# Optimization experiments

Measured on AMD Instinct MI355X. Metric: run time of the kernel, lower is better.

## Reference

```python
import jax, jax.numpy as jnp
import numpy as np

B, N, D, H = 4, 2048, 512, 8
HD = D // H  # 64


def setup_inputs() -> dict:
    key = jax.random.key(0)
    ks = jax.random.split(key, 12)
    s = 0.02
    return {
        "x": jax.random.normal(ks[0], (B, N, D), jnp.float32),
        "freqs": jax.random.normal(ks[1], (B, N, HD // 2), jnp.float32),
        # weights stored as (in, out); torch Linear applies x @ W.T + b
        "wqkv_w": jax.random.normal(ks[2], (D, 3 * D), jnp.float32) * s,
        "wqkv_b": jax.random.normal(ks[3], (3 * D,), jnp.float32) * s,
        "out_w": jax.random.normal(ks[4], (D, D), jnp.float32) * s,
        "out_b": jax.random.normal(ks[5], (D,), jnp.float32) * s,
        "ffn1_w": jax.random.normal(ks[6], (2 * D, 2 * D), jnp.float32) * s,
        "ffn1_b": jax.random.normal(ks[7], (2 * D,), jnp.float32) * s,
        "ln_g": jnp.ones((2 * D,), jnp.float32),
        "ln_b": jnp.zeros((2 * D,), jnp.float32),
        "ffn2_w": jax.random.normal(ks[8], (2 * D, D), jnp.float32) * s,
        "ffn2_b": jax.random.normal(ks[9], (D,), jnp.float32) * s,
    }


def _rope(t, cos, sin):
    # t: [B,H,N,HD]; cos/sin: [B,1,N,HD/2]
    x1, x2 = t[..., ::2], t[..., 1::2]
    return jnp.stack([x1 * cos - x2 * sin, x1 * sin + x2 * cos], axis=-1).reshape(t.shape)


def reference(x, freqs, wqkv_w, wqkv_b, out_w, out_b,
              ffn1_w, ffn1_b, ln_g, ln_b, ffn2_w, ffn2_b):
    b, n, d = x.shape
    h, hd = H, d // H
    qkv = x @ wqkv_w + wqkv_b                      # [B,N,3D]
    q, k, v = jnp.split(qkv, 3, axis=-1)
    to_heads = lambda t: t.reshape(b, n, h, hd).transpose(0, 2, 1, 3)  # [B,H,N,HD]
    q, k, v = to_heads(q), to_heads(k), to_heads(v)
    cos = jnp.cos(freqs)[:, None]                  # [B,1,N,HD/2]
    sin = jnp.sin(freqs)[:, None]
    q = _rope(q, cos, sin)
    k = _rope(k, cos, sin)
    scale = hd ** -0.5
    attn = jax.nn.softmax(jnp.einsum('bhqd,bhkd->bhqk', q, k) * scale, axis=-1)
    msg = jnp.einsum('bhqk,bhkd->bhqd', attn, v).transpose(0, 2, 1, 3).reshape(b, n, d)
    msg = msg @ out_w + out_b
    # FFN on concat([x, msg]): Linear -> LayerNorm -> GELU(exact) -> Linear
    hcat = jnp.concatenate([x, msg], axis=-1) @ ffn1_w + ffn1_b   # [B,N,2D]
    mu = hcat.mean(-1, keepdims=True)
    var = hcat.var(-1, keepdims=True)
    hcat = (hcat - mu) * jax.lax.rsqrt(var + 1e-5) * ln_g + ln_b
    hcat = jax.nn.gelu(hcat, approximate=False)
    return x + hcat @ ffn2_w + ffn2_b
```

## Files before the change

### kernel.cpp

```cpp
#include <hip/hip_runtime.h>
#include <hip/hip_bf16.h>
#include <math.h>

typedef __bf16 bf16;
typedef __bf16 bf16x2 __attribute__((ext_vector_type(2)));
typedef __bf16 bf16x4 __attribute__((ext_vector_type(4)));
typedef __bf16 bf16x8 __attribute__((ext_vector_type(8)));
typedef float f32x4 __attribute__((ext_vector_type(4)));
typedef float f32x16 __attribute__((ext_vector_type(16)));

#define MFMA16(a, b, c) __builtin_amdgcn_mfma_f32_16x16x32_bf16(a, b, c, 0, 0, 0)
#define MFMA32(a, b, c) __builtin_amdgcn_mfma_f32_32x32x16_bf16(a, b, c, 0, 0, 0)


__global__ __launch_bounds__(256) void transpose_all_kernel(
    const float* __restrict__ w0, const float* __restrict__ w1,
    const float* __restrict__ w2, const float* __restrict__ w3,
    bf16* __restrict__ d0, bf16* __restrict__ d1,
    bf16* __restrict__ d2, bf16* __restrict__ d3)
{
    const int bid = blockIdx.x;
    const float* src; bf16* dst; int R, C, bx, by;
    if (bid < 768)       { src = w0; dst = d0; R = 512;  C = 1536; int r = bid;        bx = r % 48; by = r / 48; }
    else if (bid < 1024) { src = w1; dst = d1; R = 512;  C = 512;  int r = bid - 768;  bx = r % 16; by = r / 16; }
    else if (bid < 2048) { src = w2; dst = d2; R = 1024; C = 1024; int r = bid - 1024; bx = r % 32; by = r / 32; }
    else                 { src = w3; dst = d3; R = 1024; C = 512;  int r = bid - 2048; bx = r % 16; by = r / 16; }
    __shared__ bf16 tile[32][33];
    const int tx = threadIdx.x & 31, ty = threadIdx.x >> 5;
    const int x = bx * 32 + tx;
#pragma unroll
    for (int j = 0; j < 4; j++)
        tile[ty + 8 * j][tx] = (bf16)src[(size_t)(by * 32 + ty + 8 * j) * C + x];
    __syncthreads();
    const int x2 = by * 32 + tx;
#pragma unroll
    for (int j = 0; j < 4; j++)
        dst[(size_t)(bx * 32 + ty + 8 * j) * R + x2] = tile[tx][ty + 8 * j];
}

__global__ __launch_bounds__(256) void cast_x_kernel(const float* __restrict__ x,
                                                     bf16* __restrict__ cat)
{
    int i = blockIdx.x * 256 + threadIdx.x;
    int row = i >> 7, col = (i & 127) << 2;
    const float4 v = *(const float4*)(&x[(size_t)row * 512 + col]);
    bf16x4 o; o[0] = (bf16)v.x; o[1] = (bf16)v.y; o[2] = (bf16)v.z; o[3] = (bf16)v.w;
    *(bf16x4*)(&cat[(size_t)row * 1024 + col]) = o;
}

__global__ __launch_bounds__(256) void rope_kernel(bf16* __restrict__ qb,
                                                   bf16* __restrict__ kb,
                                                   const float* __restrict__ freqs)
{
    const float SC = 0.125f * 1.44269504089f;
    const int bh = blockIdx.x >> 6, nblk = blockIdx.x & 63;
    const int g = threadIdx.x & 7, nl = threadIdx.x >> 3;
    const int n = nblk * 32 + nl;
    const int b = bh >> 3;
    const float4 f = *(const float4*)(&freqs[((size_t)b * 2048 + n) * 32 + g * 4]);
    const float cs[4] = {cosf(f.x), cosf(f.y), cosf(f.z), cosf(f.w)};
    const float sn[4] = {sinf(f.x), sinf(f.y), sinf(f.z), sinf(f.w)};
    const size_t off = ((size_t)bh * 2048 + n) * 64 + g * 8;
    bf16x8 q8 = *(bf16x8*)(qb + off);
    bf16x8 k8 = *(bf16x8*)(kb + off);
#pragma unroll
    for (int i = 0; i < 4; i++) {
        float q1 = q8[2 * i], q2 = q8[2 * i + 1];
        q8[2 * i]     = (bf16)((q1 * cs[i] - q2 * sn[i]) * SC);
        q8[2 * i + 1] = (bf16)((q1 * sn[i] + q2 * cs[i]) * SC);
        float k1 = k8[2 * i], k2 = k8[2 * i + 1];
        k8[2 * i]     = (bf16)(k1 * cs[i] - k2 * sn[i]);
        k8[2 * i + 1] = (bf16)(k1 * sn[i] + k2 * cs[i]);
    }
    *(bf16x8*)(qb + off) = q8;
    *(bf16x8*)(kb + off) = k8;
}

template <int MODE>
__global__ __launch_bounds__(256) void gemm_mfma(
    const bf16* __restrict__ A, int lda, const bf16* __restrict__ Bt,
    const float* __restrict__ bias, void* __restrict__ outv,
    const float* __restrict__ auxf, bf16* __restrict__ o1, bf16* __restrict__ o2,
    int K)
{
    const int tid = threadIdx.x;
    const int lane = tid & 63;
    const int wave = tid >> 6;
    const int wm = wave >> 1, wn = wave & 1;
    const int l15 = lane & 15, quad = lane >> 4;
    const int m0 = blockIdx.y * 128;
    const int n0 = blockIdx.x * 128;

    __shared__ bf16 As[128 * 32];
    __shared__ bf16 Bs[128 * 32];

    const int c0 = tid, c1 = tid + 256;
    const int r0 = c0 >> 2, kc0 = (c0 & 3) << 3;
    const int r1 = c1 >> 2, kc1 = (c1 & 3) << 3;

    const bf16* pA0 = &A[(size_t)(m0 + r0) * lda + kc0];
    const bf16* pA1 = &A[(size_t)(m0 + r1) * lda + kc1];
    const bf16* pB0 = &Bt[(size_t)(n0 + r0) * K + kc0];
    const bf16* pB1 = &Bt[(size_t)(n0 + r1) * K + kc1];

    const f32x4 zero = {0.f, 0.f, 0.f, 0.f};
    f32x4 acc[4][4];
#pragma unroll
    for (int i = 0; i < 4; i++)
#pragma unroll
        for (int j = 0; j < 4; j++) acc[i][j] = zero;

    bf16x8 ra0 = *(const bf16x8*)pA0;
    bf16x8 ra1 = *(const bf16x8*)pA1;
    bf16x8 rb0 = *(const bf16x8*)pB0;
    bf16x8 rb1 = *(const bf16x8*)pB1;

    for (int k0 = 0; k0 < K; k0 += 32) {
        __syncthreads();
        *(bf16x8*)(&As[c0 * 8]) = ra0;
        *(bf16x8*)(&As[c1 * 8]) = ra1;
        *(bf16x8*)(&Bs[c0 * 8]) = rb0;
        *(bf16x8*)(&Bs[c1 * 8]) = rb1;
        __syncthreads();
        if (k0 + 32 < K) {
            ra0 = *(const bf16x8*)(pA0 + k0 + 32);
            ra1 = *(const bf16x8*)(pA1 + k0 + 32);
            rb0 = *(const bf16x8*)(pB0 + k0 + 32);
            rb1 = *(const bf16x8*)(pB1 + k0 + 32);
        }
        bf16x8 af[4], bfv[4];
#pragma unroll
        for (int t = 0; t < 4; t++) {
            af[t]  = *(const bf16x8*)(&As[(wm * 64 + t * 16 + l15) * 32 + quad * 8]);
            bfv[t] = *(const bf16x8*)(&Bs[(wn * 64 + t * 16 + l15) * 32 + quad * 8]);
        }
#pragma unroll
        for (int mt = 0; mt < 4; mt++)
#pragma unroll
            for (int nt = 0; nt < 4; nt++)
                acc[mt][nt] = MFMA16(af[mt], bfv[nt], acc[mt][nt]);
    }

    const int row_base = m0 + wm * 64;
    const int col_base = n0 + wn * 64;

    if constexpr (MODE == 0) {
        const int sector = col_base >> 9;
        bf16* dstbase = (sector == 0) ? (bf16*)outv : (sector == 1 ? o1 : o2);
#pragma unroll
        for (int nt = 0; nt < 4; nt++) {
            const int col = col_base + nt * 16 + l15;
            const int cq = col & 511;
            const int h = cq >> 6, hd = cq & 63;
            const float bv = bias[col];
#pragma unroll
            for (int mt = 0; mt < 4; mt++) {
#pragma unroll
                for (int r = 0; r < 4; r++) {
                    const int mrow = row_base + mt * 16 + quad * 4 + r;
                    const int b = mrow >> 11, n = mrow & 2047;
                    dstbase[(((size_t)b * 8 + h) * 2048 + n) * 64 + hd] =
                        (bf16)(acc[mt][nt][r] + bv);
                }
            }
        }
    } else {
#pragma unroll
        for (int nt = 0; nt < 4; nt++) {
            const int col = col_base + nt * 16 + l15;
            const float bv = bias[col];
#pragma unroll
            for (int mt = 0; mt < 4; mt++) {
#pragma unroll
                for (int r = 0; r < 4; r++) {
                    const int row = row_base + mt * 16 + quad * 4 + r;
                    float v = acc[mt][nt][r] + bv;
                    if constexpr (MODE == 1) {
                        ((bf16*)outv)[(size_t)row * 1024 + 512 + col] = (bf16)v;
                    } else if constexpr (MODE == 2) {
                        ((bf16*)outv)[(size_t)row * 1024 + col] = (bf16)v;
                    } else {
                        v += auxf[(size_t)row * 512 + col];
                        ((float*)outv)[(size_t)row * 512 + col] = v;
                    }
                }
            }
        }
    }
}

__global__ __launch_bounds__(256) void attn_kernel(const bf16* __restrict__ qb,
                                                   const bf16* __restrict__ kb,
                                                   const bf16* __restrict__ vb,
                                                   bf16* __restrict__ ao)
{
    __shared__ bf16 Ks[128 * 72];
    __shared__ bf16 Vts[64 * 136];

    const int tid = threadIdx.x, lane = tid & 63, wave = tid >> 6;
    const int l31 = lane & 31, half = lane >> 5;
    const int bh = blockIdx.x >> 4, qt = blockIdx.x & 15;
    const int b = bh >> 3, h = bh & 7;
    const size_t base = (size_t)bh * 2048 * 64;
    const int m0 = qt * 128 + wave * 32;

    bf16x8 aq[4];
#pragma unroll
    for (int k4 = 0; k4 < 4; k4++)
        aq[k4] = *(const bf16x8*)(&qb[base + (size_t)(m0 + l31) * 64 + k4 * 16 + half * 8]);

    f32x16 accO[2];
#pragma unroll
    for (int i = 0; i < 16; i++) { accO[0][i] = 0.f; accO[1][i] = 0.f; }
    float lsum = 0.f;

    int krow[4], kcol[4], vpr[2], vdg[2];
#pragma unroll
    for (int i = 0; i < 4; i++) { int c = tid + i * 256; krow[i] = c >> 3; kcol[i] = (c & 7) << 3; }
#pragma unroll
    for (int i = 0; i < 2; i++) { int t = tid + i * 256; vpr[i] = t & 63; vdg[i] = t >> 6; }

    bf16x8 kreg[4], vreg0[2], vreg1[2];
    auto prefetch = [&](int key0) {
#pragma unroll
        for (int i = 0; i < 4; i++)
            kreg[i] = *(const bf16x8*)(&kb[base + (size_t)(key0 + krow[i]) * 64 + kcol[i]]);
#pragma unroll
        for (int i = 0; i < 2; i++) {
            vreg0[i] = *(const bf16x8*)(&vb[base + (size_t)(key0 + 2 * vpr[i]) * 64 + vdg[i] * 8]);
            vreg1[i] = *(const bf16x8*)(&vb[base + (size_t)(key0 + 2 * vpr[i] + 1) * 64 + vdg[i] * 8]);
        }
    };

    prefetch(0);
    for (int kt = 0; kt < 16; kt++) {
        __syncthreads();
#pragma unroll
        for (int i = 0; i < 4; i++)
            *(bf16x8*)(&Ks[krow[i] * 72 + kcol[i]]) = kreg[i];
#pragma unroll
        for (int i = 0; i < 2; i++) {
#pragma unroll
            for (int j = 0; j < 8; j++) {
                bf16x2 pr; pr[0] = vreg0[i][j]; pr[1] = vreg1[i][j];
                *(bf16x2*)(&Vts[(vdg[i] * 8 + j) * 136 + 2 * vpr[i]]) = pr;
            }
        }
        __syncthreads();
        if (kt < 15) prefetch((kt + 1) * 128);

#pragma unroll
        for (int nb = 0; nb < 4; nb++) {
            const int ko = nb * 32;
            f32x16 s;
#pragma unroll
            for (int i = 0; i < 16; i++) s[i] = 0.f;
#pragma unroll
            for (int k4 = 0; k4 < 4; k4++) {
                bf16x8 ak = *(const bf16x8*)(&Ks[(ko + l31) * 72 + k4 * 16 + half * 8]);
                s = MFMA32(ak, aq[k4], s);
            }
            float p[16];
#pragma unroll
            for (int r = 0; r < 16; r++) p[r] = exp2f(s[r]);
            lsum += (((p[0] + p[1]) + (p[2] + p[3])) + ((p[4] + p[5]) + (p[6] + p[7])))
                  + (((p[8] + p[9]) + (p[10] + p[11])) + ((p[12] + p[13]) + (p[14] + p[15])));
            unsigned pk[8];
#pragma unroll
            for (int i2 = 0; i2 < 8; i2++) {
                union { bf16x2 hh; unsigned u; } t;
                t.hh[0] = (bf16)p[2 * i2]; t.hh[1] = (bf16)p[2 * i2 + 1];
                pk[i2] = t.u;
            }
            const unsigned sa = half ? pk[0] : pk[2];
            const unsigned sb = half ? pk[1] : pk[3];
            const unsigned sc2 = half ? pk[4] : pk[6];
            const unsigned sd = half ? pk[5] : pk[7];
            const unsigned ra = (unsigned)__shfl_xor((int)sa, 32);
            const unsigned rb = (unsigned)__shfl_xor((int)sb, 32);
            const unsigned rc = (unsigned)__shfl_xor((int)sc2, 32);
            const unsigned rd = (unsigned)__shfl_xor((int)sd, 32);
            union { bf16x8 v; unsigned u[4]; } B0, B1;
            B0.u[0] = half ? ra : pk[0];
            B0.u[1] = half ? rb : pk[1];
            B0.u[2] = half ? pk[2] : ra;
            B0.u[3] = half ? pk[3] : rb;
            B1.u[0] = half ? rc : pk[4];
            B1.u[1] = half ? rd : pk[5];
            B1.u[2] = half ? pk[6] : rc;
            B1.u[3] = half ? pk[7] : rd;
#pragma unroll
            for (int dh = 0; dh < 2; dh++) {
                bf16x8 av0 = *(const bf16x8*)(&Vts[(dh * 32 + l31) * 136 + ko + half * 8]);
                bf16x8 av1 = *(const bf16x8*)(&Vts[(dh * 32 + l31) * 136 + ko + 16 + half * 8]);
                accO[dh] = MFMA32(av0, B0.v, accO[dh]);
                accO[dh] = MFMA32(av1, B1.v, accO[dh]);
            }
        }
    }

    lsum += __shfl_xor(lsum, 32);
    const float inv = 1.0f / lsum;

    const int n = m0 + l31;
    bf16* aor = ao + ((size_t)b * 2048 + n) * 512 + h * 64;
#pragma unroll
    for (int dh = 0; dh < 2; dh++) {
#pragma unroll
        for (int g = 0; g < 4; g++) {
            bf16x4 o4;
#pragma unroll
            for (int e = 0; e < 4; e++) o4[e] = (bf16)(accO[dh][g * 4 + e] * inv);
            *(bf16x4*)(&aor[dh * 32 + g * 8 + half * 4]) = o4;
        }
    }
}

__global__ __launch_bounds__(256) void ln_gelu_kernel(bf16* __restrict__ hb,
                                                      const float* __restrict__ g,
                                                      const float* __restrict__ bt)
{
    const int row = blockIdx.x, tid = threadIdx.x;
    const int lane = tid & 63, wave = tid >> 6;
    bf16* hr = hb + (size_t)row * 1024;
    bf16x4 hv = *(const bf16x4*)(&hr[tid * 4]);
    float v0 = hv[0], v1 = hv[1], v2 = hv[2], v3 = hv[3];
    float s = v0 + v1 + v2 + v3;
    float q = v0 * v0 + v1 * v1 + v2 * v2 + v3 * v3;
    for (int o = 32; o; o >>= 1) { s += __shfl_xor(s, o); q += __shfl_xor(q, o); }
    __shared__ float red[8];
    if (lane == 0) { red[wave] = s; red[4 + wave] = q; }
    __syncthreads();
    s = red[0] + red[1] + red[2] + red[3];
    q = red[4] + red[5] + red[6] + red[7];
    const float mu = s * (1.f / 1024.f);
    const float rstd = rsqrtf(q * (1.f / 1024.f) - mu * mu + 1e-5f);
    const float4 gv = *(const float4*)(&g[tid * 4]);
    const float4 bv = *(const float4*)(&bt[tid * 4]);
    float vv[4] = {v0, v1, v2, v3};
    const float gg[4] = {gv.x, gv.y, gv.z, gv.w};
    const float bb[4] = {bv.x, bv.y, bv.z, bv.w};
    bf16x4 o4;
#pragma unroll
    for (int i = 0; i < 4; i++) {
        float y = (vv[i] - mu) * rstd * gg[i] + bb[i];
        float ge = 0.5f * y * (1.0f + erff(y * 0.70710678118f));
        o4[i] = (bf16)ge;
    }
    *(bf16x4*)(&hr[tid * 4]) = o4;
}

extern "C" void kernel_launch(void* const* d_in, const int* in_sizes, int n_in,
                              void* d_out, int out_size, void* d_ws, size_t ws_size,
                              hipStream_t stream) {
    (void)in_sizes; (void)n_in; (void)out_size; (void)ws_size;
    const float* x      = (const float*)d_in[0];
    const float* freqs  = (const float*)d_in[1];
    const float* wqkv_w = (const float*)d_in[2];
    const float* wqkv_b = (const float*)d_in[3];
    const float* out_w  = (const float*)d_in[4];
    const float* out_b  = (const float*)d_in[5];
    const float* ffn1_w = (const float*)d_in[6];
    const float* ffn1_b = (const float*)d_in[7];
    const float* ln_g   = (const float*)d_in[8];
    const float* ln_b   = (const float*)d_in[9];
    const float* ffn2_w = (const float*)d_in[10];
    const float* ffn2_b = (const float*)d_in[11];
    float* out = (float*)d_out;
    bf16* ws   = (bf16*)d_ws;

    bf16* wqkv_t = ws;
    bf16* out_t  = wqkv_t + 1536 * 512;
    bf16* ffn1_t = out_t + 512 * 512;
    bf16* ffn2_t = ffn1_t + 1024 * 1024;
    bf16* cat    = ffn2_t + 512 * 1024;
    bf16* qbuf   = cat + (size_t)8192 * 1024;
    bf16* kbuf   = qbuf + (size_t)8192 * 512;
    bf16* vbuf   = kbuf + (size_t)8192 * 512;
    bf16* aobuf  = vbuf + (size_t)8192 * 512;
    bf16* hbuf   = qbuf;

    transpose_all_kernel<<<2560, 256, 0, stream>>>(wqkv_w, out_w, ffn1_w, ffn2_w,
                                                   wqkv_t, out_t, ffn1_t, ffn2_t);
    cast_x_kernel<<<4096, 256, 0, stream>>>(x, cat);

    gemm_mfma<0><<<dim3(12, 64), 256, 0, stream>>>(cat, 1024, wqkv_t, wqkv_b, qbuf, nullptr, kbuf, vbuf, 512);
    rope_kernel<<<2048, 256, 0, stream>>>(qbuf, kbuf, freqs);
    attn_kernel<<<512, 256, 0, stream>>>(qbuf, kbuf, vbuf, aobuf);
    gemm_mfma<1><<<dim3(4, 64), 256, 0, stream>>>(aobuf, 512, out_t, out_b, cat, nullptr, nullptr, nullptr, 512);
    gemm_mfma<2><<<dim3(8, 64), 256, 0, stream>>>(cat, 1024, ffn1_t, ffn1_b, hbuf, nullptr, nullptr, nullptr, 1024);
    ln_gelu_kernel<<<8192, 256, 0, stream>>>(hbuf, ln_g, ln_b);
    gemm_mfma<3><<<dim3(4, 64), 256, 0, stream>>>(hbuf, 1024, ffn2_t, ffn2_b, out, x, nullptr, nullptr, 1024);
}
```

Measured before the change: 266.3 us.

## Fold out-projection into FFN1 weights, fuse RoPE into QKV epilogue, split attention keys

Precomputes the product of the output projection and the lower half of ffn1 weights (plus a fused bias) so the activation out-projection GEMM is eliminated and attention writes straight into the concat buffer. RoPE with the softmax scale is applied inside the QKV GEMM epilogue via lane shuffles, removing the separate rope pass. Attention blocks grow to 512 threads with two waves per query group splitting keys and reducing through shared memory. Weight prep and x cast are merged into one launch; sin/cos are recomputed per element in the epilogue and bf16 rounding of the fused weight changes numerics slightly.

```diff
diff --git a/kernel.cpp b/kernel.cpp
--- a/kernel.cpp
+++ b/kernel.cpp
@@ -13,67 +13,64 @@
 #define MFMA32(a, b, c) __builtin_amdgcn_mfma_f32_32x32x16_bf16(a, b, c, 0, 0, 0)
 
 
-__global__ __launch_bounds__(256) void transpose_all_kernel(
-    const float* __restrict__ w0, const float* __restrict__ w1,
-    const float* __restrict__ w2, const float* __restrict__ w3,
-    bf16* __restrict__ d0, bf16* __restrict__ d1,
-    bf16* __restrict__ d2, bf16* __restrict__ d3)
+__global__ __launch_bounds__(256) void prep_kernel(
+    const float* __restrict__ wqkv_w, const float* __restrict__ out_w,
+    const float* __restrict__ ffn1_w, const float* __restrict__ ffn2_w,
+    const float* __restrict__ x,
+    bf16* __restrict__ wqkv_t, bf16* __restrict__ ffn2_t,
+    bf16* __restrict__ fused_t, bf16* __restrict__ ffn1bt,
+    bf16* __restrict__ out_cast, bf16* __restrict__ cat)
 {
-    const int bid = blockIdx.x;
-    const float* src; bf16* dst; int R, C, bx, by;
-    if (bid < 768)       { src = w0; dst = d0; R = 512;  C = 1536; int r = bid;        bx = r % 48; by = r / 48; }
-    else if (bid < 1024) { src = w1; dst = d1; R = 512;  C = 512;  int r = bid - 768;  bx = r % 16; by = r / 16; }
-    else if (bid < 2048) { src = w2; dst = d2; R = 1024; C = 1024; int r = bid - 1024; bx = r % 32; by = r / 32; }
-    else                 { src = w3; dst = d3; R = 1024; C = 512;  int r = bid - 2048; bx = r % 16; by = r / 16; }
+    const int bid = blockIdx.x, tid = threadIdx.x;
+    if (bid >= 2560) {
+        int i = (bid - 2560) * 256 + tid;
+        int row = i >> 7, col = (i & 127) << 2;
+        const float4 v = *(const float4*)(&x[(size_t)row * 512 + col]);
+        bf16x4 o; o[0] = (bf16)v.x; o[1] = (bf16)v.y; o[2] = (bf16)v.z; o[3] = (bf16)v.w;
+        *(bf16x4*)(&cat[(size_t)row * 1024 + col]) = o;
+        return;
+    }
+    if (bid >= 2304) {
+        int i = (bid - 2304) * 1024 + tid * 4;
+        const float4 v = *(const float4*)(&out_w[i]);
+        bf16x4 o; o[0] = (bf16)v.x; o[1] = (bf16)v.y; o[2] = (bf16)v.z; o[3] = (bf16)v.w;
+        *(bf16x4*)(&out_cast[i]) = o;
+        return;
+    }
+    const float* src; bf16* dst; int C, ldd, bx, by;
+    if (bid < 768)       { src = wqkv_w;            dst = wqkv_t;  C = 1536; ldd = 512;  int r = bid;        bx = r % 48; by = r / 48; }
+    else if (bid < 1280) { src = ffn2_w;            dst = ffn2_t;  C = 512;  ldd = 1024; int r = bid - 768;  bx = r % 16; by = r / 16; }
+    else if (bid < 1792) { src = ffn1_w;            dst = fused_t; C = 1024; ldd = 1024; int r = bid - 1280; bx = r % 32; by = r / 32; }
+    else                 { src = ffn1_w + 512*1024; dst = ffn1bt;  C = 1024; ldd = 512;  int r = bid - 1792; bx = r % 32; by = r / 32; }
     __shared__ bf16 tile[32][33];
-    const int tx = threadIdx.x & 31, ty = threadIdx.x >> 5;
-    const int x = bx * 32 + tx;
+    const int tx = tid & 31, ty = tid >> 5;
+    const int xx = bx * 32 + tx;
 #pragma unroll
     for (int j = 0; j < 4; j++)
-        tile[ty + 8 * j][tx] = (bf16)src[(size_t)(by * 32 + ty + 8 * j) * C + x];
+        tile[ty + 8 * j][tx] = (bf16)src[(size_t)(by * 32 + ty + 8 * j) * C + xx];
     __syncthreads();
     const int x2 = by * 32 + tx;
 #pragma unroll
     for (int j = 0; j < 4; j++)
-        dst[(size_t)(bx * 32 + ty + 8 * j) * R + x2] = tile[tx][ty + 8 * j];
-}
-
-__global__ __launch_bounds__(256) void cast_x_kernel(const float* __restrict__ x,
-                                                     bf16* __restrict__ cat)
+        dst[(size_t)(bx * 32 + ty + 8 * j) * ldd + x2] = tile[tx][ty + 8 * j];
+}
+
+__global__ __launch_bounds__(256) void bias_fuse_kernel(
+    const float* __restrict__ ffn1_w, const float* __restrict__ ffn1_b,
+    const float* __restrict__ out_b, float* __restrict__ bias_f)
 {
-    int i = blockIdx.x * 256 + threadIdx.x;
-    int row = i >> 7, col = (i & 127) << 2;
-    const float4 v = *(const float4*)(&x[(size_t)row * 512 + col]);
-    bf16x4 o; o[0] = (bf16)v.x; o[1] = (bf16)v.y; o[2] = (bf16)v.z; o[3] = (bf16)v.w;
-    *(bf16x4*)(&cat[(size_t)row * 1024 + col]) = o;
-}
-
-__global__ __launch_bounds__(256) void rope_kernel(bf16* __restrict__ qb,
-                                                   bf16* __restrict__ kb,
-                                                   const float* __restrict__ freqs)
-{
-    const float SC = 0.125f * 1.44269504089f;
-    const int bh = blockIdx.x >> 6, nblk = blockIdx.x & 63;
-    const int g = threadIdx.x & 7, nl = threadIdx.x >> 3;
-    const int n = nblk * 32 + nl;
-    const int b = bh >> 3;
-    const float4 f = *(const float4*)(&freqs[((size_t)b * 2048 + n) * 32 + g * 4]);
-    const float cs[4] = {cosf(f.x), cosf(f.y), cosf(f.z), cosf(f.w)};
-    const float sn[4] = {sinf(f.x), sinf(f.y), sinf(f.z), sinf(f.w)};
-    const size_t off = ((size_t)bh * 2048 + n) * 64 + g * 8;
-    bf16x8 q8 = *(bf16x8*)(qb + off);
-    bf16x8 k8 = *(bf16x8*)(kb + off);
-#pragma unroll
-    for (int i = 0; i < 4; i++) {
-        float q1 = q8[2 * i], q2 = q8[2 * i + 1];
-        q8[2 * i]     = (bf16)((q1 * cs[i] - q2 * sn[i]) * SC);
-        q8[2 * i + 1] = (bf16)((q1 * sn[i] + q2 * cs[i]) * SC);
-        float k1 = k8[2 * i], k2 = k8[2 * i + 1];
-        k8[2 * i]     = (bf16)(k1 * cs[i] - k2 * sn[i]);
-        k8[2 * i + 1] = (bf16)(k1 * sn[i] + k2 * cs[i]);
-    }
-    *(bf16x8*)(qb + off) = q8;
-    *(bf16x8*)(kb + off) = k8;
+    __shared__ float red[256];
+    const int t = threadIdx.x;
+    const int n = blockIdx.x * 64 + (t & 63);
+    const int ic = t >> 6;
+    float acc = 0.f;
+#pragma unroll 8
+    for (int i = ic * 128; i < ic * 128 + 128; i++)
+        acc += out_b[i] * ffn1_w[(size_t)(512 + i) * 1024 + n];
+    red[t] = acc;
+    __syncthreads();
+    if (t < 64)
+        bias_f[n] = ffn1_b[n] + red[t] + red[t + 64] + red[t + 128] + red[t + 192];
 }
 
 template <int MODE>
@@ -145,6 +142,7 @@
     const int col_base = n0 + wn * 64;
 
     if constexpr (MODE == 0) {
+        const float SCQ = 0.125f * 1.44269504089f;
         const int sector = col_base >> 9;
         bf16* dstbase = (sector == 0) ? (bf16*)outv : (sector == 1 ? o1 : o2);
 #pragma unroll
@@ -153,14 +151,24 @@
             const int cq = col & 511;
             const int h = cq >> 6, hd = cq & 63;
             const float bv = bias[col];
+            const int ihalf = hd >> 1;
+            const bool odd = (hd & 1) != 0;
 #pragma unroll
             for (int mt = 0; mt < 4; mt++) {
 #pragma unroll
                 for (int r = 0; r < 4; r++) {
                     const int mrow = row_base + mt * 16 + quad * 4 + r;
+                    float v = acc[mt][nt][r] + bv;
+                    float o = v;
+                    if (sector < 2) {
+                        float p = __shfl_xor(v, 1);
+                        float fr = auxf[(size_t)mrow * 32 + ihalf];
+                        float cs = cosf(fr), sn = sinf(fr);
+                        o = odd ? (p * sn + v * cs) : (v * cs - p * sn);
+                        if (sector == 0) o *= SCQ;
+                    }
                     const int b = mrow >> 11, n = mrow & 2047;
-                    dstbase[(((size_t)b * 8 + h) * 2048 + n) * 64 + hd] =
-                        (bf16)(acc[mt][nt][r] + bv);
+                    dstbase[(((size_t)b * 8 + h) * 2048 + n) * 64 + hd] = (bf16)o;
                 }
             }
         }
@@ -168,20 +176,21 @@
 #pragma unroll
         for (int nt = 0; nt < 4; nt++) {
             const int col = col_base + nt * 16 + l15;
-            const float bv = bias[col];
+            float bv = 0.f;
+            if constexpr (MODE != 4) bv = bias[col];
 #pragma unroll
             for (int mt = 0; mt < 4; mt++) {
 #pragma unroll
                 for (int r = 0; r < 4; r++) {
                     const int row = row_base + mt * 16 + quad * 4 + r;
                     float v = acc[mt][nt][r] + bv;
-                    if constexpr (MODE == 1) {
-                        ((bf16*)outv)[(size_t)row * 1024 + 512 + col] = (bf16)v;
-                    } else if constexpr (MODE == 2) {
+                    if constexpr (MODE == 2) {
                         ((bf16*)outv)[(size_t)row * 1024 + col] = (bf16)v;
-                    } else {
+                    } else if constexpr (MODE == 3) {
                         v += auxf[(size_t)row * 512 + col];
                         ((float*)outv)[(size_t)row * 512 + col] = v;
+                    } else {
+                        ((bf16*)outv)[(size_t)row * 1024 + 512 + col] = (bf16)v;
                     }
                 }
             }
@@ -189,20 +198,22 @@
     }
 }
 
-__global__ __launch_bounds__(256) void attn_kernel(const bf16* __restrict__ qb,
+__global__ __launch_bounds__(512) void attn_kernel(const bf16* __restrict__ qb,
                                                    const bf16* __restrict__ kb,
                                                    const bf16* __restrict__ vb,
-                                                   bf16* __restrict__ ao)
+                                                   bf16* __restrict__ cat)
 {
-    __shared__ bf16 Ks[128 * 72];
-    __shared__ bf16 Vts[64 * 136];
+    __shared__ __align__(16) char smem[35840];
+    bf16* Ks  = (bf16*)smem;
+    bf16* Vts = (bf16*)(smem + 128 * 72 * 2);
 
     const int tid = threadIdx.x, lane = tid & 63, wave = tid >> 6;
     const int l31 = lane & 31, half = lane >> 5;
+    const int qg = wave >> 1, kh = wave & 1;
     const int bh = blockIdx.x >> 4, qt = blockIdx.x & 15;
     const int b = bh >> 3, h = bh & 7;
     const size_t base = (size_t)bh * 2048 * 64;
-    const int m0 = qt * 128 + wave * 32;
+    const int m0 = qt * 128 + qg * 32;
 
     bf16x8 aq[4];
 #pragma unroll
@@ -214,44 +225,37 @@
     for (int i = 0; i < 16; i++) { accO[0][i] = 0.f; accO[1][i] = 0.f; }
     float lsum = 0.f;
 
-    int krow[4], kcol[4], vpr[2], vdg[2];
-#pragma unroll
-    for (int i = 0; i < 4; i++) { int c = tid + i * 256; krow[i] = c >> 3; kcol[i] = (c & 7) << 3; }
-#pragma unroll
-    for (int i = 0; i < 2; i++) { int t = tid + i * 256; vpr[i] = t & 63; vdg[i] = t >> 6; }
-
-    bf16x8 kreg[4], vreg0[2], vreg1[2];
+    int krow[2], kcol[2];
+#pragma unroll
+    for (int i = 0; i < 2; i++) { int c = tid + i * 512; krow[i] = c >> 3; kcol[i] = (c & 7) << 3; }
+    const int vpr = tid & 63, vdg = tid >> 6;
+
+    bf16x8 kreg[2], vr0, vr1;
     auto prefetch = [&](int key0) {
 #pragma unroll
-        for (int i = 0; i < 4; i++)
+        for (int i = 0; i < 2; i++)
             kreg[i] = *(const bf16x8*)(&kb[base + (size_t)(key0 + krow[i]) * 64 + kcol[i]]);
-#pragma unroll
-        for (int i = 0; i < 2; i++) {
-            vreg0[i] = *(const bf16x8*)(&vb[base + (size_t)(key0 + 2 * vpr[i]) * 64 + vdg[i] * 8]);
-            vreg1[i] = *(const bf16x8*)(&vb[base + (size_t)(key0 + 2 * vpr[i] + 1) * 64 + vdg[i] * 8]);
-        }
+        vr0 = *(const bf16x8*)(&vb[base + (size_t)(key0 + 2 * vpr) * 64 + vdg * 8]);
+        vr1 = *(const bf16x8*)(&vb[base + (size_t)(key0 + 2 * vpr + 1) * 64 + vdg * 8]);
     };
 
     prefetch(0);
     for (int kt = 0; kt < 16; kt++) {
         __syncthreads();
 #pragma unroll
-        for (int i = 0; i < 4; i++)
+        for (int i = 0; i < 2; i++)
             *(bf16x8*)(&Ks[krow[i] * 72 + kcol[i]]) = kreg[i];
 #pragma unroll
-        for (int i = 0; i < 2; i++) {
-#pragma unroll
-            for (int j = 0; j < 8; j++) {
-                bf16x2 pr; pr[0] = vreg0[i][j]; pr[1] = vreg1[i][j];
-                *(bf16x2*)(&Vts[(vdg[i] * 8 + j) * 136 + 2 * vpr[i]]) = pr;
-            }
+        for (int j = 0; j < 8; j++) {
+            bf16x2 pr; pr[0] = vr0[j]; pr[1] = vr1[j];
+            *(bf16x2*)(&Vts[(vdg * 8 + j) * 136 + 2 * vpr]) = pr;
         }
         __syncthreads();
         if (kt < 15) prefetch((kt + 1) * 128);
 
 #pragma unroll
-        for (int nb = 0; nb < 4; nb++) {
-            const int ko = nb * 32;
+        for (int nb = 0; nb < 2; nb++) {
+            const int ko = kh * 64 + nb * 32;
             f32x16 s;
 #pragma unroll
             for (int i = 0; i < 16; i++) s[i] = 0.f;
@@ -299,19 +303,31 @@
         }
     }
 
-    lsum += __shfl_xor(lsum, 32);
-    const float inv = 1.0f / lsum;
-
-    const int n = m0 + l31;
-    bf16* aor = ao + ((size_t)b * 2048 + n) * 512 + h * 64;
-#pragma unroll
-    for (int dh = 0; dh < 2; dh++) {
-#pragma unroll
-        for (int g = 0; g < 4; g++) {
-            bf16x4 o4;
-#pragma unroll
-            for (int e = 0; e < 4; e++) o4[e] = (bf16)(accO[dh][g * 4 + e] * inv);
-            *(bf16x4*)(&aor[dh * 32 + g * 8 + half * 4]) = o4;
+    __syncthreads();
+    float* red = (float*)smem + qg * 2112 + lane * 33;
+    if (kh == 1) {
+#pragma unroll
+        for (int dh = 0; dh < 2; dh++)
+#pragma unroll
+            for (int r = 0; r < 16; r++) red[dh * 16 + r] = accO[dh][r];
+        red[32] = lsum + __shfl_xor(lsum, 32);
+    }
+    __syncthreads();
+    if (kh == 0) {
+        const float lm = lsum + __shfl_xor(lsum, 32) + red[32];
+        const float inv = 1.0f / lm;
+        const int n = m0 + l31;
+        bf16* aor = cat + ((size_t)b * 2048 + n) * 1024 + 512 + h * 64;
+#pragma unroll
+        for (int dh = 0; dh < 2; dh++) {
+#pragma unroll
+            for (int g = 0; g < 4; g++) {
+                bf16x4 o4;
+#pragma unroll
+                for (int e = 0; e < 4; e++)
+                    o4[e] = (bf16)((accO[dh][g * 4 + e] + red[dh * 16 + g * 4 + e]) * inv);
+                *(bf16x4*)(&aor[dh * 32 + g * 8 + half * 4]) = o4;
+            }
         }
     }
 }
@@ -369,26 +385,26 @@
     float* out = (float*)d_out;
     bf16* ws   = (bf16*)d_ws;
 
-    bf16* wqkv_t = ws;
-    bf16* out_t  = wqkv_t + 1536 * 512;
-    bf16* ffn1_t = out_t + 512 * 512;
-    bf16* ffn2_t = ffn1_t + 1024 * 1024;
-    bf16* cat    = ffn2_t + 512 * 1024;
-    bf16* qbuf   = cat + (size_t)8192 * 1024;
-    bf16* kbuf   = qbuf + (size_t)8192 * 512;
-    bf16* vbuf   = kbuf + (size_t)8192 * 512;
-    bf16* aobuf  = vbuf + (size_t)8192 * 512;
-    bf16* hbuf   = qbuf;
-
-    transpose_all_kernel<<<2560, 256, 0, stream>>>(wqkv_w, out_w, ffn1_w, ffn2_w,
-                                                   wqkv_t, out_t, ffn1_t, ffn2_t);
-    cast_x_kernel<<<4096, 256, 0, stream>>>(x, cat);
-
-    gemm_mfma<0><<<dim3(12, 64), 256, 0, stream>>>(cat, 1024, wqkv_t, wqkv_b, qbuf, nullptr, kbuf, vbuf, 512);
-    rope_kernel<<<2048, 256, 0, stream>>>(qbuf, kbuf, freqs);
-    attn_kernel<<<512, 256, 0, stream>>>(qbuf, kbuf, vbuf, aobuf);
-    gemm_mfma<1><<<dim3(4, 64), 256, 0, stream>>>(aobuf, 512, out_t, out_b, cat, nullptr, nullptr, nullptr, 512);
-    gemm_mfma<2><<<dim3(8, 64), 256, 0, stream>>>(cat, 1024, ffn1_t, ffn1_b, hbuf, nullptr, nullptr, nullptr, 1024);
+    bf16* wqkv_t   = ws;
+    bf16* ffn2_t   = wqkv_t + 1536 * 512;
+    bf16* fused_t  = ffn2_t + 512 * 1024;
+    bf16* ffn1bt   = fused_t + 1024 * 1024;
+    bf16* out_cast = ffn1bt + 1024 * 512;
+    bf16* cat      = out_cast + 512 * 512;
+    bf16* qbuf     = cat + (size_t)8192 * 1024;
+    bf16* kbuf     = qbuf + (size_t)8192 * 512;
+    bf16* vbuf     = kbuf + (size_t)8192 * 512;
+    float* bias_f  = (float*)(vbuf + (size_t)8192 * 512);
+    bf16* hbuf     = qbuf;
+
+    prep_kernel<<<6656, 256, 0, stream>>>(wqkv_w, out_w, ffn1_w, ffn2_w, x,
+                                          wqkv_t, ffn2_t, fused_t, ffn1bt, out_cast, cat);
+    bias_fuse_kernel<<<16, 256, 0, stream>>>(ffn1_w, ffn1_b, out_b, bias_f);
+    gemm_mfma<4><<<dim3(4, 8), 256, 0, stream>>>(ffn1bt, 512, out_cast, nullptr, fused_t,
+                                                 nullptr, nullptr, nullptr, 512);
+    gemm_mfma<0><<<dim3(12, 64), 256, 0, stream>>>(cat, 1024, wqkv_t, wqkv_b, qbuf, freqs, kbuf, vbuf, 512);
+    attn_kernel<<<512, 512, 0, stream>>>(qbuf, kbuf, vbuf, cat);
+    gemm_mfma<2><<<dim3(8, 64), 256, 0, stream>>>(cat, 1024, fused_t, bias_f, hbuf, nullptr, nullptr, nullptr, 1024);
     ln_gelu_kernel<<<8192, 256, 0, stream>>>(hbuf, ln_g, ln_b);
     gemm_mfma<3><<<dim3(4, 64), 256, 0, stream>>>(hbuf, 1024, ffn2_t, ffn2_b, out, x, nullptr, nullptr, 1024);
 }
```

After: 338.3 us. 1.27x slower.
